# Kernel optimization log

Measured on AMD Instinct MI355X. Metric: run time of the kernel, lower is better.

The kernel has to match this reference:

```python
import jax, jax.numpy as jnp
import numpy as np

T, A, H, E = 16, 8, 128, 32  # steps, actions/step, hidden, embed


def setup_inputs() -> dict:
    key = jax.random.key(0)
    ks = jax.random.split(key, 16)
    n = lambda k, s: jax.random.normal(k, s, dtype=jnp.float32) * 0.1
    return {
        "old_actions": jax.random.randint(ks[0], (T,), 0, A),
        "init_input": n(ks[1], (1, E)),
        "W_ih_a": n(ks[2], (4 * H, E)), "W_hh_a": n(ks[3], (4 * H, H)),
        "b_ih_a": n(ks[4], (4 * H,)), "b_hh_a": n(ks[5], (4 * H,)),
        "heads_W": n(ks[6], (T, A, H)), "heads_b": n(ks[7], (T, A)),
        "W_ih_c": n(ks[8], (4 * H, E)), "W_hh_c": n(ks[9], (4 * H, H)),
        "b_ih_c": n(ks[10], (4 * H,)), "b_hh_c": n(ks[11], (4 * H,)),
        "critic_W": n(ks[12], (1, H)), "critic_b": n(ks[13], (1,)),
        "embed": n(ks[14], (T * A, E)),
    }


def _lstm_cell(x, h, c, W_ih, W_hh, b_ih, b_hh):
    # PyTorch LSTMCell: gate order i, f, g, o
    g = W_ih @ x + b_ih + W_hh @ h + b_hh
    i, f, gg, o = jnp.split(g, 4)
    c = jax.nn.sigmoid(f) * c + jax.nn.sigmoid(i) * jnp.tanh(gg)
    h = jax.nn.sigmoid(o) * jnp.tanh(c)
    return h, c


def reference(old_actions, init_input, W_ih_a, W_hh_a, b_ih_a, b_hh_a,
              heads_W, heads_b, W_ih_c, W_hh_c, b_ih_c, b_hh_c,
              critic_W, critic_b, embed):
    # input sequence is fully determined by the given actions
    global_idx = jnp.arange(T) * A + old_actions          # action offsets
    emb_rows = embed[global_idx]                          # [T, E]
    x_seq = jnp.concatenate([init_input, emb_rows[:-1]], axis=0)  # [T, E]

    def step(carry, xs):
        h_a, c_a, h_c, c_c = carry
        x, hw, hb, a = xs
        h_a, c_a = _lstm_cell(x, h_a, c_a, W_ih_a, W_hh_a, b_ih_a, b_hh_a)
        logits = hw @ h_a + hb                            # [A]
        logp = jax.nn.log_softmax(logits)
        probs = jnp.exp(logp)
        lp = logp[a]
        ent = -jnp.sum(probs * logp)
        h_c, c_c = _lstm_cell(x, h_c, c_c, W_ih_c, W_hh_c, b_ih_c, b_hh_c)
        val = critic_W[0] @ h_c + critic_b[0]
        return (h_a, c_a, h_c, c_c), (lp, ent, val)

    z = jnp.zeros((H,), jnp.float32)
    _, (log_probs, entropies, values) = jax.lax.scan(
        step, (z, z, z, z), (x_seq, heads_W, heads_b, old_actions))
    return log_probs, entropies, values  # each [T]
```

## Files before the change

kernel.cpp:

```cpp
#include <hip/hip_runtime.h>
#include <math.h>

#define T 16
#define A 8
#define H 128
#define E 32
#define G (4*H)

typedef _Float16 h2t __attribute__((ext_vector_type(2)));
typedef _Float16 h4t __attribute__((ext_vector_type(4)));
typedef _Float16 h8t __attribute__((ext_vector_type(8)));

__device__ __forceinline__ float sigmoidf_(float x) {
    return 1.0f / (1.0f + __expf(-x));
}
__device__ __forceinline__ float tanhf_(float x) {
    return 1.0f - 2.0f / (1.0f + __expf(2.0f * x));
}

#if __has_builtin(__builtin_amdgcn_fdot2)
#define DOT2(a, b, c) __builtin_amdgcn_fdot2((a), (b), (c), false)
#else
__device__ __forceinline__ float dot2_fb(h2t a, h2t b, float c) {
    return fmaf((float)a[0], (float)b[0], fmaf((float)a[1], (float)b[1], c));
}
#define DOT2(a, b, c) dot2_fb((a), (b), (c))
#endif

__global__ __attribute__((amdgpu_flat_work_group_size(512, 512),
                          amdgpu_waves_per_eu(2, 2)))
void ppo_ctrl_kernel(const int* __restrict__ old_actions,
                     const float* __restrict__ init_input,
                     const float* __restrict__ W_ih_a, const float* __restrict__ W_hh_a,
                     const float* __restrict__ b_ih_a, const float* __restrict__ b_hh_a,
                     const float* __restrict__ heads_W, const float* __restrict__ heads_b,
                     const float* __restrict__ W_ih_c, const float* __restrict__ W_hh_c,
                     const float* __restrict__ b_ih_c, const float* __restrict__ b_hh_c,
                     const float* __restrict__ critic_W, const float* __restrict__ critic_b,
                     const float* __restrict__ embed,
                     float* __restrict__ out)
{
    const int tid  = threadIdx.x;
    const int lane = tid & 63;
    const int wv   = tid >> 6;
    const bool actor = (blockIdx.x == 0);

    const float* W_ih = actor ? W_ih_a : W_ih_c;
    const float* W_hh = actor ? W_hh_a : W_hh_c;
    const float* b_ih = actor ? b_ih_a : b_ih_c;
    const float* b_hh = actor ? b_hh_a : b_hh_c;

    __shared__ __align__(16) _Float16 wlds[G * H];
    __shared__ __align__(16) _Float16 accx16[T][G];
    __shared__ __align__(16) _Float16 hhist[T][H];
    __shared__ __align__(16) float gates_s[G];
    __shared__ __align__(16) float x_s[T][E];
    __shared__ __align__(16) _Float16 h16[H];

    {
        int t0 = tid >> 5, e0 = tid & 31;
        float v = (t0 == 0) ? init_input[e0]
                            : embed[((t0 - 1) * A + old_actions[t0 - 1]) * E + e0];
        x_s[t0][e0] = v;
    }
    if (tid < H) h16[tid] = (_Float16)0.0f;

    #pragma unroll 4
    for (int pass = 0; pass < 32; ++pass) {
        int idx = pass * 512 + tid;
        float4 f = *(const float4*)(W_hh + idx * 4);
        unsigned r = (unsigned)idx >> 5;
        unsigned b = ((unsigned)idx & 31u) * 8u;
        unsigned addr = r * 256u + ((b & ~15u) ^ ((r & 15u) * 16u)) + (b & 8u);
        h4t p = { (_Float16)f.x, (_Float16)f.y, (_Float16)f.z, (_Float16)f.w };
        *(h4t*)((char*)wlds + addr) = p;
    }

    const float* wir = W_ih + tid * E;
    float4 wi0 = *(const float4*)(wir +  0), wi1 = *(const float4*)(wir +  4),
           wi2 = *(const float4*)(wir +  8), wi3 = *(const float4*)(wir + 12),
           wi4 = *(const float4*)(wir + 16), wi5 = *(const float4*)(wir + 20),
           wi6 = *(const float4*)(wir + 24), wi7 = *(const float4*)(wir + 28);
    const float bias = b_ih[tid] + b_hh[tid];

    __syncthreads();

    #pragma unroll 1
    for (int t = 0; t < T; ++t) {
        float s0 = 0.f, s1 = 0.f, s2 = 0.f, s3 = 0.f;
#define MACI(i) { float4 xv = *(const float4*)(&x_s[t][4*(i)]);           \
        s0 = fmaf(wi##i.x, xv.x, s0); s1 = fmaf(wi##i.y, xv.y, s1);       \
        s2 = fmaf(wi##i.z, xv.z, s2); s3 = fmaf(wi##i.w, xv.w, s3); }
        MACI(0) MACI(1) MACI(2) MACI(3) MACI(4) MACI(5) MACI(6) MACI(7)
#undef MACI
        accx16[t][tid] = (_Float16)(bias + ((s0 + s1) + (s2 + s3)));
    }

    float c_reg = 0.0f;
    const unsigned swzb = ((unsigned)(tid & 15)) * 16u;
    const char* rowbase = (const char*)wlds + tid * 256;
    const char* hbase   = (const char*)h16;

    #pragma unroll 1
    for (int t = 0; t < T; ++t) {
        float a0 = 0.f, a1 = 0.f, a2 = 0.f, a3 = 0.f;
        #pragma unroll
        for (int c = 0; c < 16; ++c) {
            h8t wq = *(const h8t*)(rowbase + (((unsigned)c * 16u) ^ swzb));
            h8t hq = *(const h8t*)(hbase + c * 16);
            a0 = DOT2(__builtin_shufflevector(wq, wq, 0, 1),
                      __builtin_shufflevector(hq, hq, 0, 1), a0);
            a1 = DOT2(__builtin_shufflevector(wq, wq, 2, 3),
                      __builtin_shufflevector(hq, hq, 2, 3), a1);
            a2 = DOT2(__builtin_shufflevector(wq, wq, 4, 5),
                      __builtin_shufflevector(hq, hq, 4, 5), a2);
            a3 = DOT2(__builtin_shufflevector(wq, wq, 6, 7),
                      __builtin_shufflevector(hq, hq, 6, 7), a3);
        }
        gates_s[tid] = (float)accx16[t][tid] + ((a0 + a1) + (a2 + a3));
        __syncthreads();

        if (tid < H) {
            float gi = gates_s[tid],       gf = gates_s[tid + H];
            float gg = gates_s[tid + 2*H], go = gates_s[tid + 3*H];
            float cn = sigmoidf_(gf) * c_reg + sigmoidf_(gi) * tanhf_(gg);
            c_reg = cn;
            float hv = sigmoidf_(go) * tanhf_(cn);
            _Float16 hf = (_Float16)hv;
            h16[tid] = hf;
            hhist[t][tid] = hf;
        }
        __syncthreads();
    }

    if (actor) {
        #pragma unroll 1
        for (int tt = wv; tt < T; tt += 8) {
            float hA = (float)hhist[tt][lane];
            float hB = (float)hhist[tt][64 + lane];
#define LOGIT(a) float l##a; {                                            \
            const float* hw = heads_W + ((tt) * A + (a)) * H;             \
            float p = fmaf(hw[lane], hA, hw[64 + lane] * hB);             \
            p += __shfl_xor(p, 1);  p += __shfl_xor(p, 2);                \
            p += __shfl_xor(p, 4);  p += __shfl_xor(p, 8);                \
            p += __shfl_xor(p, 16); p += __shfl_xor(p, 32);               \
            l##a = p + heads_b[(tt) * A + (a)]; }
            LOGIT(0) LOGIT(1) LOGIT(2) LOGIT(3)
            LOGIT(4) LOGIT(5) LOGIT(6) LOGIT(7)
#undef LOGIT
            if (lane == 0) {
                float m = fmaxf(fmaxf(fmaxf(l0, l1), fmaxf(l2, l3)),
                                fmaxf(fmaxf(l4, l5), fmaxf(l6, l7)));
                float e0 = __expf(l0 - m), e1 = __expf(l1 - m),
                      e2 = __expf(l2 - m), e3 = __expf(l3 - m),
                      e4 = __expf(l4 - m), e5 = __expf(l5 - m),
                      e6 = __expf(l6 - m), e7 = __expf(l7 - m);
                float s = ((e0 + e1) + (e2 + e3)) + ((e4 + e5) + (e6 + e7));
                float logZ = m + __logf(s);
                int act = old_actions[tt];
                float la = (act == 0) ? l0 : (act == 1) ? l1 : (act == 2) ? l2 :
                           (act == 3) ? l3 : (act == 4) ? l4 : (act == 5) ? l5 :
                           (act == 6) ? l6 : l7;
                out[tt] = la - logZ;
                float w_ = e0*(l0-logZ) + e1*(l1-logZ) + e2*(l2-logZ) + e3*(l3-logZ)
                         + e4*(l4-logZ) + e5*(l5-logZ) + e6*(l6-logZ) + e7*(l7-logZ);
                out[T + tt] = -w_ / s;
            }
        }
    } else {
        #pragma unroll 1
        for (int tt = wv; tt < T; tt += 8) {
            float hA = (float)hhist[tt][lane];
            float hB = (float)hhist[tt][64 + lane];
            float p = fmaf(critic_W[lane], hA, critic_W[64 + lane] * hB);
            p += __shfl_xor(p, 1);  p += __shfl_xor(p, 2);
            p += __shfl_xor(p, 4);  p += __shfl_xor(p, 8);
            p += __shfl_xor(p, 16); p += __shfl_xor(p, 32);
            if (lane == 0) out[2 * T + tt] = p + critic_b[0];
        }
    }
}

extern "C" void kernel_launch(void* const* d_in, const int* in_sizes, int n_in,
                              void* d_out, int out_size, void* d_ws, size_t ws_size,
                              hipStream_t stream) {
    const int*   old_actions = (const int*)  d_in[0];
    const float* init_input  = (const float*)d_in[1];
    const float* W_ih_a      = (const float*)d_in[2];
    const float* W_hh_a      = (const float*)d_in[3];
    const float* b_ih_a      = (const float*)d_in[4];
    const float* b_hh_a      = (const float*)d_in[5];
    const float* heads_W     = (const float*)d_in[6];
    const float* heads_b     = (const float*)d_in[7];
    const float* W_ih_c      = (const float*)d_in[8];
    const float* W_hh_c      = (const float*)d_in[9];
    const float* b_ih_c      = (const float*)d_in[10];
    const float* b_hh_c      = (const float*)d_in[11];
    const float* critic_W    = (const float*)d_in[12];
    const float* critic_b    = (const float*)d_in[13];
    const float* embed       = (const float*)d_in[14];
    float* out = (float*)d_out;

    ppo_ctrl_kernel<<<dim3(2), dim3(512), 0, stream>>>(
        old_actions, init_input,
        W_ih_a, W_hh_a, b_ih_a, b_hh_a,
        heads_W, heads_b,
        W_ih_c, W_hh_c, b_ih_c, b_hh_c,
        critic_W, critic_b, embed, out);
}
```

Measured before the change: 29.03 us.

## Keep recurrent weight rows in registers instead of swizzled LDS

Each thread now loads its 128-element W_hh row into sixteen fp16x8 registers instead of staging the whole matrix in swizzled LDS, so the recurrent loop reads only h from shared memory. It also skips the h·W product at t=0, keeps the input projection in fp32 LDS, and unrolls the head loops. This removes LDS traffic and bank-conflict concerns from the serial recurrence and shrinks LDS use, but raises VGPR pressure by about 64 registers per thread.

```diff
diff --git a/kernel.cpp b/kernel.cpp
--- a/kernel.cpp
+++ b/kernel.cpp
@@ -8,7 +8,6 @@
 #define G (4*H)
 
 typedef _Float16 h2t __attribute__((ext_vector_type(2)));
-typedef _Float16 h4t __attribute__((ext_vector_type(4)));
 typedef _Float16 h8t __attribute__((ext_vector_type(8)));
 
 __device__ __forceinline__ float sigmoidf_(float x) {
@@ -26,6 +25,9 @@
 }
 #define DOT2(a, b, c) dot2_fb((a), (b), (c))
 #endif
+
+#define RPT16(M) M(0) M(1) M(2) M(3) M(4) M(5) M(6) M(7) \
+                 M(8) M(9) M(10) M(11) M(12) M(13) M(14) M(15)
 
 __global__ __attribute__((amdgpu_flat_work_group_size(512, 512),
                           amdgpu_waves_per_eu(2, 2)))
@@ -50,12 +52,11 @@
     const float* b_ih = actor ? b_ih_a : b_ih_c;
     const float* b_hh = actor ? b_hh_a : b_hh_c;
 
-    __shared__ __align__(16) _Float16 wlds[G * H];
-    __shared__ __align__(16) _Float16 accx16[T][G];
-    __shared__ __align__(16) _Float16 hhist[T][H];
+    __shared__ __align__(16) float accx_s[T][G];
     __shared__ __align__(16) float gates_s[G];
     __shared__ __align__(16) float x_s[T][E];
     __shared__ __align__(16) _Float16 h16[H];
+    __shared__ __align__(16) _Float16 hhist[T][H];
 
     {
         int t0 = tid >> 5, e0 = tid & 31;
@@ -63,18 +64,18 @@
                             : embed[((t0 - 1) * A + old_actions[t0 - 1]) * E + e0];
         x_s[t0][e0] = v;
     }
-    if (tid < H) h16[tid] = (_Float16)0.0f;
-
-    #pragma unroll 4
-    for (int pass = 0; pass < 32; ++pass) {
-        int idx = pass * 512 + tid;
-        float4 f = *(const float4*)(W_hh + idx * 4);
-        unsigned r = (unsigned)idx >> 5;
-        unsigned b = ((unsigned)idx & 31u) * 8u;
-        unsigned addr = r * 256u + ((b & ~15u) ^ ((r & 15u) * 16u)) + (b & 8u);
-        h4t p = { (_Float16)f.x, (_Float16)f.y, (_Float16)f.z, (_Float16)f.w };
-        *(h4t*)((char*)wlds + addr) = p;
-    }
+
+    const float* rowp = W_hh + tid * H;
+#define LOADW(i) h8t w##i; {                                              \
+        float4 fa = *(const float4*)(rowp + 8*(i));                       \
+        float4 fb = *(const float4*)(rowp + 8*(i) + 4);                   \
+        w##i = (h8t){ (_Float16)fa.x, (_Float16)fa.y,                     \
+                      (_Float16)fa.z, (_Float16)fa.w,                     \
+                      (_Float16)fb.x, (_Float16)fb.y,                     \
+                      (_Float16)fb.z, (_Float16)fb.w };                   \
+        asm volatile("" : "+v"(w##i)); }
+    RPT16(LOADW)
+#undef LOADW
 
     const float* wir = W_ih + tid * E;
     float4 wi0 = *(const float4*)(wir +  0), wi1 = *(const float4*)(wir +  4),
@@ -93,31 +94,29 @@
         s2 = fmaf(wi##i.z, xv.z, s2); s3 = fmaf(wi##i.w, xv.w, s3); }
         MACI(0) MACI(1) MACI(2) MACI(3) MACI(4) MACI(5) MACI(6) MACI(7)
 #undef MACI
-        accx16[t][tid] = (_Float16)(bias + ((s0 + s1) + (s2 + s3)));
+        accx_s[t][tid] = bias + ((s0 + s1) + (s2 + s3));
     }
 
     float c_reg = 0.0f;
-    const unsigned swzb = ((unsigned)(tid & 15)) * 16u;
-    const char* rowbase = (const char*)wlds + tid * 256;
-    const char* hbase   = (const char*)h16;
+    const h8t* hv = (const h8t*)h16;
 
     #pragma unroll 1
     for (int t = 0; t < T; ++t) {
         float a0 = 0.f, a1 = 0.f, a2 = 0.f, a3 = 0.f;
-        #pragma unroll
-        for (int c = 0; c < 16; ++c) {
-            h8t wq = *(const h8t*)(rowbase + (((unsigned)c * 16u) ^ swzb));
-            h8t hq = *(const h8t*)(hbase + c * 16);
-            a0 = DOT2(__builtin_shufflevector(wq, wq, 0, 1),
-                      __builtin_shufflevector(hq, hq, 0, 1), a0);
-            a1 = DOT2(__builtin_shufflevector(wq, wq, 2, 3),
-                      __builtin_shufflevector(hq, hq, 2, 3), a1);
-            a2 = DOT2(__builtin_shufflevector(wq, wq, 4, 5),
-                      __builtin_shufflevector(hq, hq, 4, 5), a2);
-            a3 = DOT2(__builtin_shufflevector(wq, wq, 6, 7),
-                      __builtin_shufflevector(hq, hq, 6, 7), a3);
-        }
-        gates_s[tid] = (float)accx16[t][tid] + ((a0 + a1) + (a2 + a3));
+        if (t != 0) {
+#define MACC(i) { h8t hq = hv[i];                                          \
+            a0 = DOT2(__builtin_shufflevector(w##i, w##i, 0, 1),           \
+                      __builtin_shufflevector(hq,  hq,  0, 1), a0);        \
+            a1 = DOT2(__builtin_shufflevector(w##i, w##i, 2, 3),           \
+                      __builtin_shufflevector(hq,  hq,  2, 3), a1);        \
+            a2 = DOT2(__builtin_shufflevector(w##i, w##i, 4, 5),           \
+                      __builtin_shufflevector(hq,  hq,  4, 5), a2);        \
+            a3 = DOT2(__builtin_shufflevector(w##i, w##i, 6, 7),           \
+                      __builtin_shufflevector(hq,  hq,  6, 7), a3); }
+            RPT16(MACC)
+#undef MACC
+        }
+        gates_s[tid] = accx_s[t][tid] + ((a0 + a1) + (a2 + a3));
         __syncthreads();
 
         if (tid < H) {
@@ -125,8 +124,8 @@
             float gg = gates_s[tid + 2*H], go = gates_s[tid + 3*H];
             float cn = sigmoidf_(gf) * c_reg + sigmoidf_(gi) * tanhf_(gg);
             c_reg = cn;
-            float hv = sigmoidf_(go) * tanhf_(cn);
-            _Float16 hf = (_Float16)hv;
+            float hvv = sigmoidf_(go) * tanhf_(cn);
+            _Float16 hf = (_Float16)hvv;
             h16[tid] = hf;
             hhist[t][tid] = hf;
         }
@@ -134,17 +133,18 @@
     }
 
     if (actor) {
-        #pragma unroll 1
-        for (int tt = wv; tt < T; tt += 8) {
+        #pragma unroll
+        for (int rep = 0; rep < 2; ++rep) {
+            const int tt = wv + rep * 8;
             float hA = (float)hhist[tt][lane];
             float hB = (float)hhist[tt][64 + lane];
 #define LOGIT(a) float l##a; {                                            \
-            const float* hw = heads_W + ((tt) * A + (a)) * H;             \
+            const float* hw = heads_W + (tt * A + (a)) * H;               \
             float p = fmaf(hw[lane], hA, hw[64 + lane] * hB);             \
             p += __shfl_xor(p, 1);  p += __shfl_xor(p, 2);                \
             p += __shfl_xor(p, 4);  p += __shfl_xor(p, 8);                \
             p += __shfl_xor(p, 16); p += __shfl_xor(p, 32);               \
-            l##a = p + heads_b[(tt) * A + (a)]; }
+            l##a = p + heads_b[tt * A + (a)]; }
             LOGIT(0) LOGIT(1) LOGIT(2) LOGIT(3)
             LOGIT(4) LOGIT(5) LOGIT(6) LOGIT(7)
 #undef LOGIT
@@ -168,8 +168,9 @@
             }
         }
     } else {
-        #pragma unroll 1
-        for (int tt = wv; tt < T; tt += 8) {
+        #pragma unroll
+        for (int rep = 0; rep < 2; ++rep) {
+            const int tt = wv + rep * 8;
             float hA = (float)hhist[tt][lane];
             float hB = (float)hhist[tt][64 + lane];
             float p = fmaf(critic_W[lane], hA, critic_W[64 + lane] * hB);
```

Result: slower. 31.40 us (+8.2%).
